# Performance work log

Hardware: AMD Instinct MI355X
Metric: run time of the kernel (lower is better)

The kernel has to match this reference:

```python
import jax, jax.numpy as jnp
import numpy as np

B, L, V, E_ENC, D_DEC, E_EMB = 256, 128, 4096, 1024, 1024, 512


def _lin(key, out_f, in_f, scale=0.02):
    k1, k2 = jax.random.split(key)
    return (jax.random.normal(k1, (out_f, in_f), jnp.float32) * scale,
            jax.random.normal(k2, (out_f,), jnp.float32) * scale)


def setup_inputs() -> dict:
    key = jax.random.key(0)
    ks = jax.random.split(key, 12)
    x = jax.random.normal(ks[0], (B, 1, V), jnp.float32)
    hidden = jax.random.normal(ks[1], (1, B, D_DEC), jnp.float32)
    enc_output = jax.random.normal(ks[2], (B, L, E_ENC), jnp.float32)
    W1_w, W1_b = _lin(ks[3], D_DEC, E_ENC)
    W2_w, W2_b = _lin(ks[4], D_DEC, D_DEC)
    V_w, V_b = _lin(ks[5], 1, D_DEC)
    out2emb_w, out2emb_b = _lin(ks[6], E_EMB, V)
    gru_wi, gru_bi = _lin(ks[7], 3 * D_DEC, E_EMB + E_ENC)
    gru_wh, gru_bh = _lin(ks[8], 3 * D_DEC, D_DEC)
    fc1_w, fc1_b = _lin(ks[9], E_EMB, D_DEC)
    fc2_w, fc2_b = _lin(ks[10], V, E_EMB)
    return dict(x=x, hidden=hidden, enc_output=enc_output,
                W1_w=W1_w, W1_b=W1_b, W2_w=W2_w, W2_b=W2_b, V_w=V_w, V_b=V_b,
                out2emb_w=out2emb_w, out2emb_b=out2emb_b,
                gru_wi=gru_wi, gru_wh=gru_wh, gru_bi=gru_bi, gru_bh=gru_bh,
                fc1_w=fc1_w, fc1_b=fc1_b, fc2_w=fc2_w, fc2_b=fc2_b)


def reference(x, hidden, enc_output, W1_w, W1_b, W2_w, W2_b, V_w, V_b,
              out2emb_w, out2emb_b, gru_wi, gru_wh, gru_bi, gru_bh,
              fc1_w, fc1_b, fc2_w, fc2_b):
    # --- Bahdanau additive attention ---
    h_t = hidden[-1][:, None, :]                                   # (B,1,dec)
    score = jnp.tanh(enc_output @ W1_w.T + W1_b + h_t @ W2_w.T + W2_b)  # (B,L,dec)
    attn = jax.nn.softmax(score @ V_w.T + V_b, axis=1)             # (B,L,1)
    context = jnp.sum(attn * enc_output, axis=1)                   # (B,enc)
    # --- embed previous output distribution ---
    x_emb = x @ out2emb_w.T + out2emb_b                            # (B,1,emb)
    rnn_in = jnp.concatenate([context[:, None, :], x_emb], -1)[:, 0, :]  # (B,emb+enc)
    # --- single GRU step (PyTorch gate layout r,z,n) ---
    h0 = hidden[0]
    gi = rnn_in @ gru_wi.T + gru_bi
    gh = h0 @ gru_wh.T + gru_bh
    ir, iz, inn = jnp.split(gi, 3, axis=-1)
    hr, hz, hn = jnp.split(gh, 3, axis=-1)
    r = jax.nn.sigmoid(ir + hr)
    z = jax.nn.sigmoid(iz + hz)
    n = jnp.tanh(inn + r * hn)
    h_new = (1.0 - z) * n + z * h0                                 # (B,dec)
    # --- output MLP ---
    out = jnp.tanh(h_new @ fc1_w.T + fc1_b) @ fc2_w.T + fc2_b      # (B,vocab)
    return out, h_new[None], attn
```

## Files before the change

kernel.cpp:

```cpp
#include <hip/hip_runtime.h>
#include <math.h>


#define B_   256
#define L_   128
#define V_   4096
#define ENC_ 1024
#define DEC_ 1024
#define EMB_ 512
#define MB_  1048576ull

typedef __bf16 bf16;
typedef __bf16 bf16x8 __attribute__((ext_vector_type(8)));
typedef __bf16 bf16x4 __attribute__((ext_vector_type(4)));
typedef float  f32x4  __attribute__((ext_vector_type(4)));

__device__ __forceinline__ float fast_tanh(float x) {
  float e = __builtin_amdgcn_exp2f(x * 2.88539008177792681472f);
  return 1.0f - 2.0f * __builtin_amdgcn_rcpf(e + 1.0f);
}
__device__ __forceinline__ float fast_sigmoid(float x) {
  return __builtin_amdgcn_rcpf(1.0f + __builtin_amdgcn_exp2f(-1.44269504088896f * x));
}

__device__ __forceinline__ void cp16(const void* g, void* l) {
  __builtin_amdgcn_global_load_lds(
      (const __attribute__((address_space(1))) void*)g,
      (__attribute__((address_space(3))) void*)l,
      16, 0, 0);
}

__device__ __forceinline__ bf16x8 ld8f(const float* f) {
  f32x4 a = *(const f32x4*)f;
  f32x4 b = *(const f32x4*)(f + 4);
  bf16x8 r;
  r[0] = (bf16)a[0]; r[1] = (bf16)a[1]; r[2] = (bf16)a[2]; r[3] = (bf16)a[3];
  r[4] = (bf16)b[0]; r[5] = (bf16)b[1]; r[6] = (bf16)b[2]; r[7] = (bf16)b[3];
  return r;
}


__device__ __forceinline__ void gemm64_pipe(
    const float* __restrict__ A, const float* __restrict__ Brow,
    int strideA, int strideB, int kbeg, int kend, int row0,
    bf16* As, bf16* Bs, f32x4 acc[4])
{
  const int t   = threadIdx.x;
  const int lane = t & 63, w = t >> 6, q = lane >> 4, c16 = lane & 15;
  const int sr  = t >> 3, lb = t & 7;

  bf16x8 va[2], vb[2];
#pragma unroll
  for (int ch = 0; ch < 2; ch++) {
    int r    = ch * 32 + sr;
    int gcol = kbeg + ((lb ^ (r & 7)) << 3);
    va[ch] = ld8f(A    + (size_t)(row0 + r) * strideA + gcol);
    vb[ch] = ld8f(Brow + (size_t)r * strideB + gcol);
  }

  for (int k0 = kbeg; k0 < kend; k0 += 64) {
#pragma unroll
    for (int ch = 0; ch < 2; ch++) {
      *(bf16x8*)&As[ch * 2048 + t * 8] = va[ch];
      *(bf16x8*)&Bs[ch * 2048 + t * 8] = vb[ch];
    }
    __syncthreads();
    if (k0 + 64 < kend) {
#pragma unroll
      for (int ch = 0; ch < 2; ch++) {
        int r    = ch * 32 + sr;
        int gcol = k0 + 64 + ((lb ^ (r & 7)) << 3);
        va[ch] = ld8f(A    + (size_t)(row0 + r) * strideA + gcol);
        vb[ch] = ld8f(Brow + (size_t)r * strideB + gcol);
      }
    }
#pragma unroll
    for (int kkb = 0; kkb < 8; kkb += 4) {
      int rb = w * 16 + c16;
      bf16x8 bfr = *(const bf16x8*)&Bs[rb * 64 + (((kkb + q) ^ (rb & 7)) << 3)];
#pragma unroll
      for (int i = 0; i < 4; i++) {
        int ra = i * 16 + c16;
        bf16x8 af = *(const bf16x8*)&As[ra * 64 + (((kkb + q) ^ (ra & 7)) << 3)];
        acc[i] = __builtin_amdgcn_mfma_f32_16x16x32_bf16(af, bfr, acc[i], 0, 0, 0);
      }
    }
    __syncthreads();
  }
}

__global__ __launch_bounds__(256) void setup_k(
    const float* __restrict__ hidden, const float* __restrict__ W2,
    const float* __restrict__ wh, const float* __restrict__ W1_b,
    const float* __restrict__ W2_b, const float* __restrict__ gbh,
    const float* __restrict__ x, const float* __restrict__ o2e,
    const float* __restrict__ enc, const float* __restrict__ W1,
    const float* __restrict__ wi, const float* __restrict__ fc1w,
    const float* __restrict__ fc2w,
    bf16* __restrict__ enc_bf, bf16* __restrict__ W1_bf,
    bf16* __restrict__ wi_bf, bf16* __restrict__ fc1_bf,
    bf16* __restrict__ fc2_bf,
    bf16* __restrict__ u, bf16* __restrict__ gh, float* __restrict__ xe4)
{
  __shared__ __align__(16) bf16 As[64 * 64];
  __shared__ __align__(16) bf16 Bs[64 * 64];

  const int bid = blockIdx.x;
  const int t   = threadIdx.x;

  if (bid >= 384) {
    for (int c = bid - 384; c < 10240; c += 1664) {
      const float* src; bf16* dst; int blk;
      if      (c < 8192) { src = enc;  dst = enc_bf; blk = c; }
      else if (c < 8448) { src = W1;   dst = W1_bf;  blk = c - 8192; }
      else if (c < 9600) { src = wi;   dst = wi_bf;  blk = c - 8448; }
      else if (c < 9728) { src = fc1w; dst = fc1_bf; blk = c - 9600; }
      else               { src = fc2w; dst = fc2_bf; blk = c - 9728; }
      const size_t base = (size_t)blk * 4096 + t * 16;
      const float* s = src + base;
      bf16* d = dst + base;
      *(bf16x8*)(d)     = ld8f(s);
      *(bf16x8*)(d + 8) = ld8f(s + 8);
    }
    return;
  }

  const int lane = t & 63, w = t >> 6, q = lane >> 4, c16 = lane & 15;
  f32x4 acc[4] = {};

  if (bid < 256) {
    const int row0 = (bid >> 6) * 64;
    const int col0 = (bid & 63) * 64;
    const bool isU = (col0 < 1024);
    const float* Brow = isU ? (W2 + (size_t)col0 * 1024)
                            : (wh + (size_t)(col0 - 1024) * 1024);
    gemm64_pipe(hidden, Brow, 1024, 1024, 0, 1024, row0, As, Bs, acc);

    const int gc = col0 + w * 16 + c16;
    float bias = isU ? (W1_b[gc] + W2_b[gc]) : gbh[gc - 1024];
#pragma unroll
    for (int i = 0; i < 4; i++) {
      int gr0 = row0 + i * 16 + q * 4;
#pragma unroll
      for (int r = 0; r < 4; r++) {
        float v = acc[i][r] + bias;
        if (isU) u[(size_t)(gr0 + r) * 1024 + gc] = (bf16)v;
        else     gh[(size_t)(gr0 + r) * 3072 + (gc - 1024)] = (bf16)v;
      }
    }
  } else {
    const int i3   = bid - 256;
    const int col0 = (i3 & 7) * 64;
    const int row0 = ((i3 >> 3) & 3) * 64;
    const int z    = i3 >> 5;
    gemm64_pipe(x, o2e + (size_t)col0 * 4096, 4096, 4096,
                z * 1024, z * 1024 + 1024, row0, As, Bs, acc);

    const int gc = col0 + w * 16 + c16;
    float* out = xe4 + (size_t)z * 131072;
#pragma unroll
    for (int i = 0; i < 4; i++) {
      int gr0 = row0 + i * 16 + q * 4;
#pragma unroll
      for (int r = 0; r < 4; r++)
        out[(size_t)(gr0 + r) * 512 + gc] = acc[i][r];
    }
  }
}

__device__ __forceinline__ void stage_half(
    const bf16* __restrict__ src, bf16* dst, int grow0, int k0, int t)
{
  const int sr = t >> 3, lb = t & 7;
#pragma unroll
  for (int ch = 0; ch < 2; ch++) {
    int r    = ch * 64 + sr;
    int gcol = k0 + ((lb ^ (r & 7)) << 3);
    cp16(src + (size_t)(grow0 + r) * 1024 + gcol, dst + r * 64 + lb * 8);
  }
}

#define BAR()   __builtin_amdgcn_s_barrier()
#define FENCE() asm volatile("" ::: "memory")
#define VM2()   asm volatile("s_waitcnt vmcnt(2)" ::: "memory")
#define VM4()   asm volatile("s_waitcnt vmcnt(4)" ::: "memory")
#define PHASE_END() { FENCE(); BAR(); FENCE(); }

#define RD_A4(dst, base, ib, kq)                                            \
  _Pragma("unroll") for (int i = 0; i < 4; i++) {                           \
    const int ra = ra_base + ((ib) + i) * 16;                               \
    dst[i] = *(const bf16x8*)&(base)[ra * 64 + (((kq) ^ (ra & 7)) << 3)];   \
  }
#define RD_B4(dst, base, kq)                                                \
  _Pragma("unroll") for (int j = 0; j < 4; j++) {                           \
    const int rb = rb_base + j * 16;                                        \
    dst[j] = *(const bf16x8*)&(base)[rb * 64 + (((kq) ^ (rb & 7)) << 3)];   \
  }
#define MFMA16(ib, afv, bv)                                                 \
  __builtin_amdgcn_s_setprio(1);                                            \
  _Pragma("unroll") for (int i = 0; i < 4; i++)                             \
    _Pragma("unroll") for (int j = 0; j < 4; j++)                           \
      acc[(ib) + i][j] = __builtin_amdgcn_mfma_f32_16x16x32_bf16(           \
          afv[i], bv[j], acc[(ib) + i][j], 0, 0, 0);                        \
  __builtin_amdgcn_s_setprio(0);

__global__ __launch_bounds__(512, 2) void score_8p(
    const bf16* __restrict__ A,
    const bf16* __restrict__ Bw,
    const bf16* __restrict__ u,
    const float* __restrict__ Vw,
    float* __restrict__ e_part)
{
  __shared__ __align__(16) bf16 sA0[16384];
  __shared__ __align__(16) bf16 sA1[16384];
  __shared__ __align__(16) bf16 sB0[16384];
  __shared__ __align__(16) bf16 sB1[16384];
  __shared__ float s_part[4][256];

  const int t = threadIdx.x;
  const int wg  = blockIdx.x;
  const int swz = (wg & 7) * 64 + (wg >> 3);
  const int bx  = swz & 3;
  const int by  = swz >> 2;
  const int row0 = by * 256;
  const int col0 = bx * 256;

  const int lane = t & 63, w = t >> 6;
  const int wm = w >> 2, wn = w & 3;
  const int q = lane >> 4, c16 = lane & 15;
  const int rb_base = wn * 64 + c16;
  const int ra_base = wm * 128 + c16;

  bf16x8 afA[4], afB[4], b0[4], b1[4];
  f32x4 acc[8][4] = {};

  stage_half(A,  sA0,        row0,       0,  t);
  stage_half(A,  sA0 + 8192, row0 + 128, 0,  t);
  stage_half(Bw, sB0,        col0,       0,  t);
  stage_half(Bw, sB0 + 8192, col0 + 128, 0,  t);
  stage_half(Bw, sB1,        col0,       64, t);
  stage_half(Bw, sB1 + 8192, col0 + 128, 64, t);
  VM4();
  PHASE_END();
  RD_A4(afA, sA0, 0, q);
  RD_B4(b0, sB0, q);

  for (int k = 0; k < 8; ++k) {
    const int e = 2 * k, o = 2 * k + 1;
    const bool nl = (k < 7);

    RD_A4(afB, sA0, 0, 4 + q);
    RD_B4(b1, sB0, 4 + q);
    stage_half(A, sA1, row0, o * 64, t);
    MFMA16(0, afA, b0);
    PHASE_END();

    RD_A4(afA, sA0, 4, q);
    stage_half(A, sA1 + 8192, row0 + 128, o * 64, t);
    MFMA16(0, afB, b1);
    PHASE_END();

    RD_A4(afB, sA0, 4, 4 + q);
    if (nl) stage_half(Bw, sB0, col0, (e + 2) * 64, t);
    MFMA16(4, afA, b0);
    VM2();
    PHASE_END();

    RD_A4(afA, sA1, 0, q);
    RD_B4(b0, sB1, q);
    if (nl) stage_half(Bw, sB0 + 8192, col0 + 128, (e + 2) * 64, t);
    MFMA16(4, afB, b1);
    PHASE_END();

    RD_A4(afB, sA1, 0, 4 + q);
    RD_B4(b1, sB1, 4 + q);
    if (nl) stage_half(A, sA0, row0, (e + 2) * 64, t);
    MFMA16(0, afA, b0);
    PHASE_END();

    RD_A4(afA, sA1, 4, q);
    if (nl) stage_half(A, sA0 + 8192, row0 + 128, (e + 2) * 64, t);
    MFMA16(0, afB, b1);
    PHASE_END();

    RD_A4(afB, sA1, 4, 4 + q);
    if (nl) stage_half(Bw, sB1, col0, (o + 2) * 64, t);
    MFMA16(4, afA, b0);
    VM2();
    PHASE_END();

    if (nl) {
      RD_A4(afA, sA0, 0, q);
      RD_B4(b0, sB0, q);
      stage_half(Bw, sB1 + 8192, col0 + 128, (o + 2) * 64, t);
    }
    MFMA16(4, afB, b1);
    PHASE_END();
  }

  const int b = by * 2 + wm;
  float uc[4], vw[4];
#pragma unroll
  for (int j = 0; j < 4; j++) {
    const int gc = col0 + wn * 64 + j * 16 + c16;
    uc[j] = (float)u[b * 1024 + gc];
    vw[j] = Vw[gc];
  }
  float rsum[8][4];
#pragma unroll
  for (int i = 0; i < 8; i++) {
#pragma unroll
    for (int r = 0; r < 4; r++) {
      float v = 0.0f;
#pragma unroll
      for (int j = 0; j < 4; j++)
        v += fast_tanh(acc[i][j][r] + uc[j]) * vw[j];
      v += __shfl_xor(v, 1);
      v += __shfl_xor(v, 2);
      v += __shfl_xor(v, 4);
      v += __shfl_xor(v, 8);
      rsum[i][r] = v;
    }
  }
#pragma unroll
  for (int i = 0; i < 8; i++)
#pragma unroll
    for (int r = 0; r < 4; r++)
      if (c16 == 0) s_part[wn][wm * 128 + i * 16 + q * 4 + r] = rsum[i][r];
  __syncthreads();
  if (t < 256)
    e_part[(size_t)bx * 32768 + row0 + t] =
        s_part[0][t] + s_part[1][t] + s_part[2][t] + s_part[3][t];
}

__global__ __launch_bounds__(256) void softmax_f(
    const float* __restrict__ e_part,
    const bf16* __restrict__ enc,
    const float* __restrict__ xe4,
    const float* __restrict__ o2eb,
    float* __restrict__ attn_out,
    bf16* __restrict__ rnn_in)
{
  const int b = blockIdx.x;
  const int t = threadIdx.x;
  __shared__ float se[128];

  if (t < 128) {
    float s = 0.0f;
#pragma unroll
    for (int cb = 0; cb < 4; cb++) s += e_part[(size_t)cb * 32768 + b * 128 + t];
    se[t] = s;
  }
  __syncthreads();

  float m = -1e30f;
  for (int l = 0; l < 128; l++) m = fmaxf(m, se[l]);
  float sum = 0.0f;
  for (int l = 0; l < 128; l++) sum += expf(se[l] - m);
  float inv = 1.0f / sum;
  __syncthreads();
  if (t < 128) {
    float p = expf(se[t] - m) * inv;
    attn_out[b * 128 + t] = p;
    se[t] = p;
  }
  __syncthreads();

  float a0[4] = {}, a1[4] = {}, a2[4] = {}, a3[4] = {};
  const bf16* ep = enc + (size_t)b * L_ * ENC_ + t * 4;
#pragma unroll 1
  for (int l = 0; l < 32; l++) {
#pragma unroll
    for (int s = 0; s < 4; s++) {
      float p = se[l + s * 32];
      bf16x4 v = *(const bf16x4*)(ep + (size_t)(l + s * 32) * ENC_);
      a0[s] += p * (float)v[0]; a1[s] += p * (float)v[1];
      a2[s] += p * (float)v[2]; a3[s] += p * (float)v[3];
    }
  }
  bf16x4 o;
  o[0] = (bf16)(a0[0] + a0[1] + a0[2] + a0[3]);
  o[1] = (bf16)(a1[0] + a1[1] + a1[2] + a1[3]);
  o[2] = (bf16)(a2[0] + a2[1] + a2[2] + a2[3]);
  o[3] = (bf16)(a3[0] + a3[1] + a3[2] + a3[3]);
  *(bf16x4*)(rnn_in + (size_t)b * 1536 + t * 4) = o;

#pragma unroll
  for (int jj = 0; jj < 2; jj++) {
    int j = jj * 256 + t;
    float v = o2eb[j];
#pragma unroll
    for (int z = 0; z < 4; z++) v += xe4[(size_t)z * 131072 + b * 512 + j];
    rnn_in[(size_t)b * 1536 + 1024 + j] = (bf16)v;
  }
}

template <int ACT, int OUTF32>
__global__ __launch_bounds__(256) void gemm_f(
    const bf16* __restrict__ A, const bf16* __restrict__ Bw,
    const float* __restrict__ bias1,
    void* __restrict__ C, int K, int out_ld)
{
  __shared__ __align__(16) bf16 As[64 * 64];
  __shared__ __align__(16) bf16 Bs[64 * 64];

  const int t    = threadIdx.x;
  const int lane = t & 63;
  const int w    = t >> 6;
  const int q    = lane >> 4;
  const int c16  = lane & 15;
  const int sr   = t >> 3;
  const int lb   = t & 7;
  const int row0 = blockIdx.y * 64;
  const int col0 = blockIdx.x * 64;

  f32x4 acc[4] = {};

  for (int k0 = 0; k0 < K; k0 += 64) {
#pragma unroll
    for (int ch = 0; ch < 2; ch++) {
      int r    = ch * 32 + sr;
      int gcol = k0 + ((lb ^ (r & 7)) << 3);
      cp16(A  + (size_t)(row0 + r) * K + gcol, &As[ch * 2048 + t * 8]);
      cp16(Bw + (size_t)(col0 + r) * K + gcol, &Bs[ch * 2048 + t * 8]);
    }
    __syncthreads();
#pragma unroll
    for (int kkb = 0; kkb < 8; kkb += 4) {
      int rb = w * 16 + c16;
      bf16x8 bfr = *(const bf16x8*)&Bs[rb * 64 + (((kkb + q) ^ (rb & 7)) << 3)];
#pragma unroll
      for (int i = 0; i < 4; i++) {
        int ra = i * 16 + c16;
        bf16x8 af = *(const bf16x8*)&As[ra * 64 + (((kkb + q) ^ (ra & 7)) << 3)];
        acc[i] = __builtin_amdgcn_mfma_f32_16x16x32_bf16(af, bfr, acc[i], 0, 0, 0);
      }
    }
    __syncthreads();
  }

  const int gc = col0 + w * 16 + c16;
  float bias = bias1[gc];
#pragma unroll
  for (int i = 0; i < 4; i++) {
    int gr0 = row0 + i * 16 + q * 4;
#pragma unroll
    for (int r = 0; r < 4; r++) {
      float v = acc[i][r] + bias;
      if (ACT == 1) v = fast_tanh(v);
      size_t off = (size_t)(gr0 + r) * out_ld + gc;
      if (OUTF32) ((float*)C)[off] = v;
      else        ((bf16*)C)[off] = (bf16)v;
    }
  }
}

__global__ __launch_bounds__(256) void gru_f(
    const bf16* __restrict__ gi, const bf16* __restrict__ gh,
    const float* __restrict__ h0,
    float* __restrict__ hnew_out, bf16* __restrict__ hnew_i)
{
  int idx = blockIdx.x * 256 + threadIdx.x;
  int b = idx >> 10, d = idx & 1023;
  const bf16* gib = gi + b * 3072;
  const bf16* ghb = gh + b * 3072;
  float ir = (float)gib[d], iz = (float)gib[1024 + d], in = (float)gib[2048 + d];
  float hr = (float)ghb[d], hz = (float)ghb[1024 + d], hn = (float)ghb[2048 + d];
  float r = fast_sigmoid(ir + hr);
  float z = fast_sigmoid(iz + hz);
  float n = fast_tanh(in + r * hn);
  float h = (1.0f - z) * n + z * h0[idx];
  hnew_out[idx] = h;
  hnew_i[idx]   = (bf16)h;
}

extern "C" void kernel_launch(void* const* d_in, const int* in_sizes, int n_in,
                              void* d_out, int out_size, void* d_ws, size_t ws_size,
                              hipStream_t stream) {
  const float* x      = (const float*)d_in[0];
  const float* hidden = (const float*)d_in[1];
  const float* enc    = (const float*)d_in[2];
  const float* W1_w   = (const float*)d_in[3];
  const float* W1_b   = (const float*)d_in[4];
  const float* W2_w   = (const float*)d_in[5];
  const float* W2_b   = (const float*)d_in[6];
  const float* V_w    = (const float*)d_in[7];
  const float* o2e_w  = (const float*)d_in[9];
  const float* o2e_b  = (const float*)d_in[10];
  const float* gru_wi = (const float*)d_in[11];
  const float* gru_wh = (const float*)d_in[12];
  const float* gru_bi = (const float*)d_in[13];
  const float* gru_bh = (const float*)d_in[14];
  const float* fc1_w  = (const float*)d_in[15];
  const float* fc1_b  = (const float*)d_in[16];
  const float* fc2_w  = (const float*)d_in[17];
  const float* fc2_b  = (const float*)d_in[18];

  float* out_main = (float*)d_out;
  float* out_h    = out_main + (size_t)B_ * V_;
  float* out_attn = out_h + (size_t)B_ * DEC_;

  char* ws = (char*)d_ws;
  bf16*  enc_bf  = (bf16*)(ws);
  bf16*  W1_bf   = (bf16*)(ws + 64 * MB_);
  bf16*  wi_bf   = (bf16*)(ws + 66 * MB_);
  bf16*  fc1_bf  = (bf16*)(ws + 75 * MB_);
  bf16*  fc2_bf  = (bf16*)(ws + 76 * MB_);
  bf16*  u_bf    = (bf16*)(ws + 80 * MB_);
  bf16*  gh_bf   = (bf16*)(ws + 80 * MB_ + 524288);
  float* e_part  = (float*)(ws + 82 * MB_);
  bf16*  gi_bf   = (bf16*)(ws + 82 * MB_ + 524288);
  bf16*  rnn_in  = (bf16*)(ws + 84 * MB_);
  bf16*  tbuf    = (bf16*)(ws + 84 * MB_ + 786432);
  bf16*  hnew_bf = (bf16*)(ws + 85 * MB_);
  float* xe4     = (float*)(ws + 85 * MB_ + 524288);

  setup_k<<<2048, 256, 0, stream>>>(
      hidden, W2_w, gru_wh, W1_b, W2_b, gru_bh, x, o2e_w,
      enc, W1_w, gru_wi, fc1_w, fc2_w,
      enc_bf, W1_bf, wi_bf, fc1_bf, fc2_bf, u_bf, gh_bf, xe4);

  score_8p<<<512, 512, 0, stream>>>(enc_bf, W1_bf, u_bf, V_w, e_part);

  softmax_f<<<B_, 256, 0, stream>>>(e_part, enc_bf, xe4, o2e_b, out_attn, rnn_in);

  gemm_f<0, 0><<<dim3(48, 4), 256, 0, stream>>>(rnn_in, wi_bf, gru_bi, gi_bf, 1536, 3072);

  gru_f<<<(B_ * DEC_) / 256, 256, 0, stream>>>(gi_bf, gh_bf, hidden, out_h, hnew_bf);

  gemm_f<1, 0><<<dim3(8, 4), 256, 0, stream>>>(hnew_bf, fc1_bf, fc1_b, tbuf, 1024, 512);

  gemm_f<0, 1><<<dim3(64, 4), 256, 0, stream>>>(tbuf, fc2_bf, fc2_b, out_main, 512, 4096);
}
```

Measured before the change: 424.1 us.

## Fuse fp32-to-bf16 conversion of enc and W1 into score GEMM register staging

Drops the separate pass that converts enc_output and W1 to bf16 in the setup kernel. The score GEMM now loads fp32 tiles straight into registers, converts them, and writes swizzled bf16 to LDS, replacing the async cp16 pipeline with a register-staged prefetch one phase ahead. The softmax/context kernel reads fp32 enc directly and rounds each value through bf16 to keep the numerics unchanged. This saves writing and re-reading 64MB of bf16 enc, but the GEMM now reads twice as many bytes from fp32 and needs more registers for staging.

```diff
diff --git a/kernel.cpp b/kernel.cpp
--- a/kernel.cpp
+++ b/kernel.cpp
@@ -94,10 +94,8 @@
     const float* __restrict__ wh, const float* __restrict__ W1_b,
     const float* __restrict__ W2_b, const float* __restrict__ gbh,
     const float* __restrict__ x, const float* __restrict__ o2e,
-    const float* __restrict__ enc, const float* __restrict__ W1,
     const float* __restrict__ wi, const float* __restrict__ fc1w,
     const float* __restrict__ fc2w,
-    bf16* __restrict__ enc_bf, bf16* __restrict__ W1_bf,
     bf16* __restrict__ wi_bf, bf16* __restrict__ fc1_bf,
     bf16* __restrict__ fc2_bf,
     bf16* __restrict__ u, bf16* __restrict__ gh, float* __restrict__ xe4)
@@ -109,19 +107,16 @@
   const int t   = threadIdx.x;
 
   if (bid >= 384) {
-    for (int c = bid - 384; c < 10240; c += 1664) {
-      const float* src; bf16* dst; int blk;
-      if      (c < 8192) { src = enc;  dst = enc_bf; blk = c; }
-      else if (c < 8448) { src = W1;   dst = W1_bf;  blk = c - 8192; }
-      else if (c < 9600) { src = wi;   dst = wi_bf;  blk = c - 8448; }
-      else if (c < 9728) { src = fc1w; dst = fc1_bf; blk = c - 9600; }
-      else               { src = fc2w; dst = fc2_bf; blk = c - 9728; }
-      const size_t base = (size_t)blk * 4096 + t * 16;
-      const float* s = src + base;
-      bf16* d = dst + base;
-      *(bf16x8*)(d)     = ld8f(s);
-      *(bf16x8*)(d + 8) = ld8f(s + 8);
-    }
+    int i = bid - 384;
+    const float* src; bf16* dst; int blk;
+    if      (i < 1152) { src = wi;   dst = wi_bf;  blk = i; }
+    else if (i < 1280) { src = fc1w; dst = fc1_bf; blk = i - 1152; }
+    else               { src = fc2w; dst = fc2_bf; blk = i - 1280; }
+    const size_t base = (size_t)blk * 4096 + t * 16;
+    const float* s = src + base;
+    bf16* d = dst + base;
+    *(bf16x8*)(d)     = ld8f(s);
+    *(bf16x8*)(d + 8) = ld8f(s + 8);
     return;
   }
 
@@ -168,22 +163,32 @@
   }
 }
 
-__device__ __forceinline__ void stage_half(
-    const bf16* __restrict__ src, bf16* dst, int grow0, int k0, int t)
+__device__ __forceinline__ void load_half(
+    const float* __restrict__ src, int grow0, int k0, int t, f32x4 lv[4])
 {
   const int sr = t >> 3, lb = t & 7;
+  const float* p0 = src + (size_t)(grow0 + sr) * 1024 + k0 + lb * 8;
+  const float* p1 = src + (size_t)(grow0 + 64 + sr) * 1024 + k0 + lb * 8;
+  lv[0] = *(const f32x4*)p0; lv[1] = *(const f32x4*)(p0 + 4);
+  lv[2] = *(const f32x4*)p1; lv[3] = *(const f32x4*)(p1 + 4);
+}
+
+__device__ __forceinline__ void write_half(bf16* dst, int t, const f32x4 lv[4])
+{
+  const int sr = t >> 3, lb = t & 7;
 #pragma unroll
   for (int ch = 0; ch < 2; ch++) {
-    int r    = ch * 64 + sr;
-    int gcol = k0 + ((lb ^ (r & 7)) << 3);
-    cp16(src + (size_t)(grow0 + r) * 1024 + gcol, dst + r * 64 + lb * 8);
+    const int r = ch * 64 + sr;
+    const f32x4 a = lv[ch * 2], b = lv[ch * 2 + 1];
+    bf16x8 o;
+    o[0] = (bf16)a[0]; o[1] = (bf16)a[1]; o[2] = (bf16)a[2]; o[3] = (bf16)a[3];
+    o[4] = (bf16)b[0]; o[5] = (bf16)b[1]; o[6] = (bf16)b[2]; o[7] = (bf16)b[3];
+    *(bf16x8*)&dst[r * 64 + ((lb ^ (r & 7)) << 3)] = o;
   }
 }
 
 #define BAR()   __builtin_amdgcn_s_barrier()
 #define FENCE() asm volatile("" ::: "memory")
-#define VM2()   asm volatile("s_waitcnt vmcnt(2)" ::: "memory")
-#define VM4()   asm volatile("s_waitcnt vmcnt(4)" ::: "memory")
 #define PHASE_END() { FENCE(); BAR(); FENCE(); }
 
 #define RD_A4(dst, base, ib, kq)                                            \
@@ -204,9 +209,9 @@
           afv[i], bv[j], acc[(ib) + i][j], 0, 0, 0);                        \
   __builtin_amdgcn_s_setprio(0);
 
-__global__ __launch_bounds__(512, 2) void score_8p(
-    const bf16* __restrict__ A,
-    const bf16* __restrict__ Bw,
+__global__ __launch_bounds__(512, 2) void score_rs(
+    const float* __restrict__ A,
+    const float* __restrict__ Bw,
     const bf16* __restrict__ u,
     const float* __restrict__ Vw,
     float* __restrict__ e_part)
@@ -231,70 +236,90 @@
   const int rb_base = wn * 64 + c16;
   const int ra_base = wm * 128 + c16;
 
-  bf16x8 afA[4], afB[4], b0[4], b1[4];
+  bf16x8 af[4], b0[4], b1[4];
+  f32x4 rA[4], rB[4];
   f32x4 acc[8][4] = {};
 
-  stage_half(A,  sA0,        row0,       0,  t);
-  stage_half(A,  sA0 + 8192, row0 + 128, 0,  t);
-  stage_half(Bw, sB0,        col0,       0,  t);
-  stage_half(Bw, sB0 + 8192, col0 + 128, 0,  t);
-  stage_half(Bw, sB1,        col0,       64, t);
-  stage_half(Bw, sB1 + 8192, col0 + 128, 64, t);
-  VM4();
-  PHASE_END();
-  RD_A4(afA, sA0, 0, q);
-  RD_B4(b0, sB0, q);
+  load_half(A,  row0,        0,  t, rA);
+  load_half(A,  row0 + 128,  0,  t, rB);  write_half(sA0,        t, rA);
+  load_half(Bw, col0,        0,  t, rA);  write_half(sA0 + 8192, t, rB);
+  load_half(Bw, col0 + 128,  0,  t, rB);  write_half(sB0,        t, rA);
+  load_half(Bw, col0,        64, t, rA);  write_half(sB0 + 8192, t, rB);
+  load_half(Bw, col0 + 128,  64, t, rB);  write_half(sB1,        t, rA);
+  load_half(A,  row0,        64, t, rA);  write_half(sB1 + 8192, t, rB);
+  asm volatile("s_waitcnt lgkmcnt(0)" ::: "memory");
+  BAR(); FENCE();
 
   for (int k = 0; k < 8; ++k) {
     const int e = 2 * k, o = 2 * k + 1;
     const bool nl = (k < 7);
 
-    RD_A4(afB, sA0, 0, 4 + q);
-    RD_B4(b1, sB0, 4 + q);
-    stage_half(A, sA1, row0, o * 64, t);
-    MFMA16(0, afA, b0);
-    PHASE_END();
-
-    RD_A4(afA, sA0, 4, q);
-    stage_half(A, sA1 + 8192, row0 + 128, o * 64, t);
-    MFMA16(0, afB, b1);
-    PHASE_END();
-
-    RD_A4(afB, sA0, 4, 4 + q);
-    if (nl) stage_half(Bw, sB0, col0, (e + 2) * 64, t);
-    MFMA16(4, afA, b0);
-    VM2();
-    PHASE_END();
-
-    RD_A4(afA, sA1, 0, q);
-    RD_B4(b0, sB1, q);
-    if (nl) stage_half(Bw, sB0 + 8192, col0 + 128, (e + 2) * 64, t);
-    MFMA16(4, afB, b1);
-    PHASE_END();
-
-    RD_A4(afB, sA1, 0, 4 + q);
-    RD_B4(b1, sB1, 4 + q);
-    if (nl) stage_half(A, sA0, row0, (e + 2) * 64, t);
-    MFMA16(0, afA, b0);
-    PHASE_END();
-
-    RD_A4(afA, sA1, 4, q);
-    if (nl) stage_half(A, sA0 + 8192, row0 + 128, (e + 2) * 64, t);
-    MFMA16(0, afB, b1);
-    PHASE_END();
-
-    RD_A4(afB, sA1, 4, 4 + q);
-    if (nl) stage_half(Bw, sB1, col0, (o + 2) * 64, t);
-    MFMA16(4, afA, b0);
-    VM2();
+    load_half(A, row0 + 128, o * 64, t, rB);
+    write_half(sA1, t, rA);
+    FENCE();
+    RD_A4(af, sA0, 0, q); RD_B4(b0, sB0, q);
+    MFMA16(0, af, b0);
+    PHASE_END();
+
+    if (nl) load_half(Bw, col0, (e + 2) * 64, t, rA);
+    write_half(sA1 + 8192, t, rB);
+    FENCE();
+    RD_A4(af, sA0, 0, 4 + q); RD_B4(b1, sB0, 4 + q);
+    MFMA16(0, af, b1);
     PHASE_END();
 
     if (nl) {
-      RD_A4(afA, sA0, 0, q);
-      RD_B4(b0, sB0, q);
-      stage_half(Bw, sB1 + 8192, col0 + 128, (o + 2) * 64, t);
-    }
-    MFMA16(4, afB, b1);
+      load_half(Bw, col0 + 128, (e + 2) * 64, t, rB);
+      write_half(sB0, t, rA);
+    }
+    FENCE();
+    RD_A4(af, sA0, 4, q);
+    MFMA16(4, af, b0);
+    PHASE_END();
+
+    if (nl) {
+      load_half(A, row0, (e + 2) * 64, t, rA);
+      write_half(sB0 + 8192, t, rB);
+    }
+    FENCE();
+    RD_A4(af, sA0, 4, 4 + q);
+    MFMA16(4, af, b1);
+    PHASE_END();
+
+    if (nl) {
+      load_half(A, row0 + 128, (e + 2) * 64, t, rB);
+      write_half(sA0, t, rA);
+    }
+    FENCE();
+    RD_A4(af, sA1, 0, q); RD_B4(b0, sB1, q);
+    MFMA16(0, af, b0);
+    PHASE_END();
+
+    if (nl) {
+      load_half(Bw, col0, (o + 2) * 64, t, rA);
+      write_half(sA0 + 8192, t, rB);
+    }
+    FENCE();
+    RD_A4(af, sA1, 0, 4 + q); RD_B4(b1, sB1, 4 + q);
+    MFMA16(0, af, b1);
+    PHASE_END();
+
+    if (nl) {
+      load_half(Bw, col0 + 128, (o + 2) * 64, t, rB);
+      write_half(sB1, t, rA);
+    }
+    FENCE();
+    RD_A4(af, sA1, 4, q);
+    MFMA16(4, af, b0);
+    PHASE_END();
+
+    if (nl) {
+      load_half(A, row0, (o + 2) * 64, t, rA);
+      write_half(sB1 + 8192, t, rB);
+    }
+    FENCE();
+    RD_A4(af, sA1, 4, 4 + q);
+    MFMA16(4, af, b1);
     PHASE_END();
   }
 
@@ -335,7 +360,7 @@
 
 __global__ __launch_bounds__(256) void softmax_f(
     const float* __restrict__ e_part,
-    const bf16* __restrict__ enc,
+    const float* __restrict__ enc,
     const float* __restrict__ xe4,
     const float* __restrict__ o2eb,
     float* __restrict__ attn_out,
@@ -367,15 +392,15 @@
   __syncthreads();
 
   float a0[4] = {}, a1[4] = {}, a2[4] = {}, a3[4] = {};
-  const bf16* ep = enc + (size_t)b * L_ * ENC_ + t * 4;
+  const float* ep = enc + (size_t)b * L_ * ENC_ + t * 4;
 #pragma unroll 1
   for (int l = 0; l < 32; l++) {
 #pragma unroll
     for (int s = 0; s < 4; s++) {
       float p = se[l + s * 32];
-      bf16x4 v = *(const bf16x4*)(ep + (size_t)(l + s * 32) * ENC_);
-      a0[s] += p * (float)v[0]; a1[s] += p * (float)v[1];
-      a2[s] += p * (float)v[2]; a3[s] += p * (float)v[3];
+      f32x4 v = *(const f32x4*)(ep + (size_t)(l + s * 32) * ENC_);
+      a0[s] += p * (float)(bf16)v[0]; a1[s] += p * (float)(bf16)v[1];
+      a2[s] += p * (float)(bf16)v[2]; a3[s] += p * (float)(bf16)v[3];
     }
   }
   bf16x4 o;
@@ -501,28 +526,26 @@
   float* out_attn = out_h + (size_t)B_ * DEC_;
 
   char* ws = (char*)d_ws;
-  bf16*  enc_bf  = (bf16*)(ws);
-  bf16*  W1_bf   = (bf16*)(ws + 64 * MB_);
-  bf16*  wi_bf   = (bf16*)(ws + 66 * MB_);
-  bf16*  fc1_bf  = (bf16*)(ws + 75 * MB_);
-  bf16*  fc2_bf  = (bf16*)(ws + 76 * MB_);
-  bf16*  u_bf    = (bf16*)(ws + 80 * MB_);
-  bf16*  gh_bf   = (bf16*)(ws + 80 * MB_ + 524288);
-  float* e_part  = (float*)(ws + 82 * MB_);
-  bf16*  gi_bf   = (bf16*)(ws + 82 * MB_ + 524288);
-  bf16*  rnn_in  = (bf16*)(ws + 84 * MB_);
-  bf16*  tbuf    = (bf16*)(ws + 84 * MB_ + 786432);
-  bf16*  hnew_bf = (bf16*)(ws + 85 * MB_);
-  float* xe4     = (float*)(ws + 85 * MB_ + 524288);
-
-  setup_k<<<2048, 256, 0, stream>>>(
+  bf16*  wi_bf   = (bf16*)(ws);
+  bf16*  fc1_bf  = (bf16*)(ws + 9 * MB_);
+  bf16*  fc2_bf  = (bf16*)(ws + 10 * MB_);
+  bf16*  u_bf    = (bf16*)(ws + 14 * MB_);
+  bf16*  gh_bf   = (bf16*)(ws + 14 * MB_ + 524288);
+  float* e_part  = (float*)(ws + 16 * MB_);
+  bf16*  gi_bf   = (bf16*)(ws + 16 * MB_ + 524288);
+  bf16*  rnn_in  = (bf16*)(ws + 18 * MB_);
+  bf16*  tbuf    = (bf16*)(ws + 18 * MB_ + 786432);
+  bf16*  hnew_bf = (bf16*)(ws + 19 * MB_);
+  float* xe4     = (float*)(ws + 19 * MB_ + 524288);
+
+  setup_k<<<2176, 256, 0, stream>>>(
       hidden, W2_w, gru_wh, W1_b, W2_b, gru_bh, x, o2e_w,
-      enc, W1_w, gru_wi, fc1_w, fc2_w,
-      enc_bf, W1_bf, wi_bf, fc1_bf, fc2_bf, u_bf, gh_bf, xe4);
-
-  score_8p<<<512, 512, 0, stream>>>(enc_bf, W1_bf, u_bf, V_w, e_part);
-
-  softmax_f<<<B_, 256, 0, stream>>>(e_part, enc_bf, xe4, o2e_b, out_attn, rnn_in);
+      gru_wi, fc1_w, fc2_w,
+      wi_bf, fc1_bf, fc2_bf, u_bf, gh_bf, xe4);
+
+  score_rs<<<512, 512, 0, stream>>>(enc, W1_w, u_bf, V_w, e_part);
+
+  softmax_f<<<B_, 256, 0, stream>>>(e_part, enc, xe4, o2e_b, out_attn, rnn_in);
 
   gemm_f<0, 0><<<dim3(48, 4), 256, 0, stream>>>(rnn_in, wi_bf, gru_bi, gi_bf, 1536, 3072);
 
```

After: 409.5 us. -3.4%, faster.
